# Kernel optimization log

Measured on AMD Instinct MI355X. Metric: run time of the kernel, lower is better.

The kernel has to match this reference:

```python
import jax, jax.numpy as jnp
import numpy as np

EMBED_DIM = 1024
HEAD_DIM = 64


def setup_inputs() -> dict:
    key = jax.random.key(0)
    ks = jax.random.split(key, 7)
    s_in = EMBED_DIM ** -0.5  # torch Linear default init scale
    x = jax.random.normal(ks[0], (4, 4096, EMBED_DIM), dtype=jnp.float32)
    Wk = jax.random.uniform(ks[1], (HEAD_DIM, EMBED_DIM), jnp.float32, -s_in, s_in)
    bk = jax.random.uniform(ks[2], (HEAD_DIM,), jnp.float32, -s_in, s_in)
    Wq = jax.random.uniform(ks[3], (HEAD_DIM, EMBED_DIM), jnp.float32, -s_in, s_in)
    bq = jax.random.uniform(ks[4], (HEAD_DIM,), jnp.float32, -s_in, s_in)
    Wv = jax.random.uniform(ks[5], (HEAD_DIM, EMBED_DIM), jnp.float32, -s_in, s_in)
    bv = jax.random.uniform(ks[6], (HEAD_DIM,), jnp.float32, -s_in, s_in)
    return {"x": x, "Wq": Wq, "bq": bq, "Wk": Wk, "bk": bk, "Wv": Wv, "bv": bv}


def reference(x, Wq, bq, Wk, bk, Wv, bv):
    # torch Linear: y = x @ W.T + b
    q = jnp.einsum('btc,dc->btd', x, Wq) + bq  # [B,T,D]
    k = jnp.einsum('btc,dc->btd', x, Wk) + bk
    v = jnp.einsum('btc,dc->btd', x, Wv) + bv
    scale = HEAD_DIM ** -0.5
    # NOTE: original divides by scale (multiplies by sqrt(head_dim)) -- faithful
    scores = jnp.einsum('btd,bsd->bts', q, k) / scale  # [B,T,T]
    attn_weights = jax.nn.softmax(scores, axis=-1)
    return jnp.einsum('bts,bsd->btd', attn_weights, v)
```

## Files before the change

kernel.cpp:

```cpp
#include <hip/hip_runtime.h>

#define BATCH 4
#define SEQ   4096
#define CDIM  1024
#define DDIM  64
#define NROW  (BATCH * SEQ)
#define SPA   70
#define NSPL  8

typedef _Float16 f16;
typedef _Float16 f16x8 __attribute__((ext_vector_type(8)));
typedef _Float16 f16x4 __attribute__((ext_vector_type(4)));
typedef __fp16   h16x2 __attribute__((ext_vector_type(2)));
typedef float    f32x4 __attribute__((ext_vector_type(4)));

#define MFMA32(a, b, c) __builtin_amdgcn_mfma_f32_16x16x32_f16((a), (b), (c), 0, 0, 0)
#define MFMA16(a, b, c) __builtin_amdgcn_mfma_f32_16x16x16f16((a), (b), (c), 0, 0, 0)

#define GLDS(g, l)                                                            \
  __builtin_amdgcn_global_load_lds((const __attribute__((address_space(1))) void*)(g), \
                                   (__attribute__((address_space(3))) void*)(l), 16, 0, 0)

#define QSCALE 11.5415603f

__device__ inline f16x8 cvt8(f32x4 a, f32x4 b) {
  h16x2 p0 = __builtin_amdgcn_cvt_pkrtz(a[0], a[1]);
  h16x2 p1 = __builtin_amdgcn_cvt_pkrtz(a[2], a[3]);
  h16x2 p2 = __builtin_amdgcn_cvt_pkrtz(b[0], b[1]);
  h16x2 p3 = __builtin_amdgcn_cvt_pkrtz(b[2], b[3]);
  f16x8 r;
  r[0] = p0[0]; r[1] = p0[1]; r[2] = p1[0]; r[3] = p1[1];
  r[4] = p2[0]; r[5] = p2[1]; r[6] = p3[0]; r[7] = p3[1];
  return r;
}

__device__ inline f16x4 cvt4(float a, float b, float c, float d) {
  h16x2 lo = __builtin_amdgcn_cvt_pkrtz(a, b);
  h16x2 hi = __builtin_amdgcn_cvt_pkrtz(c, d);
  f16x4 r;
  r[0] = lo[0]; r[1] = lo[1]; r[2] = hi[0]; r[3] = hi[1];
  return r;
}

__global__ __launch_bounds__(256) void prep_w_kernel(const float* __restrict__ Wq,
                                                     const float* __restrict__ Wk,
                                                     const float* __restrict__ Wv,
                                                     f16* __restrict__ wf) {
  const int i = (blockIdx.x * 256 + threadIdx.x) * 4;
  f32x4 a = *(const f32x4*)(Wq + i);
  f32x4 b = *(const f32x4*)(Wk + i);
  f32x4 c = *(const f32x4*)(Wv + i);
  *(f16x4*)(wf + i)          = cvt4(a[0], a[1], a[2], a[3]);
  *(f16x4*)(wf + 65536 + i)  = cvt4(b[0], b[1], b[2], b[3]);
  *(f16x4*)(wf + 131072 + i) = cvt4(c[0], c[1], c[2], c[3]);
}

__global__ __launch_bounds__(256, 1) void proj_kernel(const float* __restrict__ x,
                                                      const f16* __restrict__ wf,
                                                      const float* __restrict__ bq,
                                                      const float* __restrict__ bk,
                                                      const float* __restrict__ bv,
                                                      f16* __restrict__ qs,
                                                      f16* __restrict__ ks,
                                                      f16* __restrict__ vT) {
  __shared__ __attribute__((aligned(16))) float xb[2][4096];
  __shared__ __attribute__((aligned(16))) f16 wb[2][12288];
  const int tid = threadIdx.x, lane = tid & 63, w = tid >> 6;
  const int n = lane & 15, quad = lane >> 4;
  const int rowbase = blockIdx.x * 64;
  const int row0w = rowbase + w * 16;

  const float* xsrc[4];
#pragma unroll
  for (int i = 0; i < 4; ++i) {
    const int c2 = i >> 1, h = i & 1;
    xsrc[i] = x + (size_t)(row0w + n) * CDIM + c2 * 32 + quad * 8 + h * 4;
  }
  const f16* wsrc[6];
#pragma unroll
  for (int i = 0; i < 6; ++i) {
    const int e = w * 6 + i;
    const int c2e = e / 12, mt = e % 12;
    wsrc[i] = wf + (size_t)((mt >> 2) * 64 + (mt & 3) * 16 + n) * CDIM + c2e * 32 + quad * 8;
  }

  f32x4 acc[12];
#pragma unroll
  for (int t_ = 0; t_ < 12; ++t_) acc[t_] = (f32x4){0.f, 0.f, 0.f, 0.f};

  auto issue = [&](int ck, int b) {
#pragma unroll
    for (int i = 0; i < 4; ++i)
      GLDS(xsrc[i] + ck * 64, &xb[b][(w * 4 + i) * 256]);
#pragma unroll
    for (int i = 0; i < 6; ++i)
      GLDS(wsrc[i] + ck * 64, &wb[b][(w * 6 + i) * 512]);
  };

  issue(0, 0);
  __syncthreads();
  for (int ck = 0; ck < 16; ++ck) {
    const int b = ck & 1;
    if (ck + 1 < 16) issue(ck + 1, b ^ 1);
#pragma unroll
    for (int c2 = 0; c2 < 2; ++c2) {
      const f32x4 x0 = *(const f32x4*)&xb[b][(w * 4 + c2 * 2) * 256 + lane * 4];
      const f32x4 x1 = *(const f32x4*)&xb[b][(w * 4 + c2 * 2 + 1) * 256 + lane * 4];
      const f16x8 a = cvt8(x0, x1);
#pragma unroll
      for (int mt = 0; mt < 12; ++mt) {
        const f16x8 bf = *(const f16x8*)&wb[b][(c2 * 12 + mt) * 512 + lane * 8];
        acc[mt] = MFMA32(a, bf, acc[mt]);
      }
    }
    __syncthreads();
  }

  const float* bias_p[3] = {bq, bk, bv};
#pragma unroll
  for (int mat = 0; mat < 3; ++mat)
#pragma unroll
    for (int tile = 0; tile < 4; ++tile) {
      const int d = tile * 16 + n;
      const float bias = bias_p[mat][d];
      const int r0 = row0w + quad * 4;
      f32x4 a = acc[mat * 4 + tile];
      if (mat == 0) {
#pragma unroll
        for (int r = 0; r < 4; ++r)
          qs[(size_t)(r0 + r) * DDIM + d] = (f16)((a[r] + bias) * QSCALE);
      } else if (mat == 1) {
#pragma unroll
        for (int r = 0; r < 4; ++r)
          ks[(size_t)(r0 + r) * DDIM + d] = (f16)(a[r] + bias);
      } else {
        const int bb = r0 >> 12;
        const int t = r0 & (SEQ - 1);
        *(f16x4*)(vT + (size_t)(bb * 64 + d) * SEQ + t) =
            cvt4(a[0] + bias, a[1] + bias, a[2] + bias, a[3] + bias);
      }
    }
}

template <int NSPLIT>
__global__ __launch_bounds__(256, 4) void attn_kernel(const f16* __restrict__ qs,
                                                      const f16* __restrict__ ks,
                                                      const f16* __restrict__ vT,
                                                      float* __restrict__ outp,
                                                      f16* __restrict__ pacc,
                                                      float* __restrict__ pm,
                                                      float* __restrict__ pl) {
  __shared__ __attribute__((aligned(16))) f16 lk[64][SPA];
  __shared__ __attribute__((aligned(16))) f16 lv[64][SPA];
  const int tid = threadIdx.x, lane = tid & 63, w = tid >> 6;
  const int n = lane & 15, quad = lane >> 4;
  const int split = blockIdx.x % NSPLIT;
  const int rowblk = blockIdx.x / NSPLIT;
  const int row0 = rowblk * 128 + w * 32;
  const int bb = row0 >> 12;
  const int kbase = split * (SEQ / NSPLIT);
  const int NC = SEQ / NSPLIT / 64;

  const f16* kb = ks + (size_t)bb * SEQ * DDIM;
  const f16* vb = vT + (size_t)bb * DDIM * SEQ;

  const int srow = tid >> 2;
  const int scol = (tid & 3) * 16;
  const f16* kgp = kb + (size_t)(kbase + srow) * DDIM + scol;
  const f16* vgp = vb + (size_t)srow * SEQ + kbase + scol;

  f16x8 qf[2][2];
#pragma unroll
  for (int g = 0; g < 2; ++g)
#pragma unroll
    for (int hh = 0; hh < 2; ++hh)
      qf[g][hh] = *(const f16x8*)(qs + (size_t)(row0 + g * 16 + n) * DDIM + hh * 32 + quad * 8);

  f32x4 acc[2][4];
  float m[2] = {-1e30f, -1e30f}, ll[2] = {0.f, 0.f};
#pragma unroll
  for (int g = 0; g < 2; ++g)
#pragma unroll
    for (int t = 0; t < 4; ++t) acc[g][t] = (f32x4){0.f, 0.f, 0.f, 0.f};

  f16x8 kr0, kr1, vr0, vr1;
  auto gload = [&](int c) {
    const f16* kp = kgp + (size_t)c * 64 * DDIM;
    kr0 = *(const f16x8*)kp;
    kr1 = *(const f16x8*)(kp + 8);
    const f16* vp = vgp + c * 64;
    vr0 = *(const f16x8*)vp;
    vr1 = *(const f16x8*)(vp + 8);
  };

  gload(0);
  for (int c = 0; c < NC; ++c) {
    *(f16x8*)&lk[srow][scol] = kr0;
    *(f16x8*)&lk[srow][scol + 8] = kr1;
    *(f16x8*)&lv[srow][scol] = vr0;
    *(f16x8*)&lv[srow][scol + 8] = vr1;
    __syncthreads();
    if (c + 1 < NC) gload(c + 1);

    f32x4 s[2][4];
#pragma unroll
    for (int st = 0; st < 4; ++st) {
      const f16x8 klo = *(const f16x8*)&lk[st * 16 + n][quad * 8];
      const f16x8 khi = *(const f16x8*)&lk[st * 16 + n][32 + quad * 8];
#pragma unroll
      for (int g = 0; g < 2; ++g) {
        f32x4 z = (f32x4){0.f, 0.f, 0.f, 0.f};
        z = MFMA32(klo, qf[g][0], z);
        s[g][st] = MFMA32(khi, qf[g][1], z);
      }
    }

    f16x4 pq[2][4];
#pragma unroll
    for (int g = 0; g < 2; ++g) {
      f32x4 mx;
#pragma unroll
      for (int r = 0; r < 4; ++r)
        mx[r] = fmaxf(fmaxf(s[g][0][r], s[g][1][r]), fmaxf(s[g][2][r], s[g][3][r]));
      float mloc = fmaxf(fmaxf(mx[0], mx[1]), fmaxf(mx[2], mx[3]));
      mloc = fmaxf(mloc, __shfl_xor(mloc, 16));
      mloc = fmaxf(mloc, __shfl_xor(mloc, 32));
      const float mnew = fmaxf(m[g], mloc);
      const float alpha = __builtin_amdgcn_exp2f(m[g] - mnew);
      m[g] = mnew;
      float psum = 0.f;
#pragma unroll
      for (int st = 0; st < 4; ++st) {
        f32x4 p;
#pragma unroll
        for (int r = 0; r < 4; ++r) p[r] = __builtin_amdgcn_exp2f(s[g][st][r] - mnew);
        psum += (p[0] + p[1]) + (p[2] + p[3]);
        pq[g][st] = cvt4(p[0], p[1], p[2], p[3]);
      }
      ll[g] = ll[g] * alpha + psum;
#pragma unroll
      for (int t = 0; t < 4; ++t) acc[g][t] *= alpha;
    }

#pragma unroll
    for (int t = 0; t < 4; ++t)
#pragma unroll
      for (int st = 0; st < 4; ++st) {
        const f16x4 va = *(const f16x4*)&lv[t * 16 + n][st * 16 + quad * 4];
        acc[0][t] = MFMA16(va, pq[0][st], acc[0][t]);
        acc[1][t] = MFMA16(va, pq[1][st], acc[1][t]);
      }
    __syncthreads();
  }

  float lred[2];
#pragma unroll
  for (int g = 0; g < 2; ++g) {
    float l = ll[g];
    l += __shfl_xor(l, 16);
    l += __shfl_xor(l, 32);
    lred[g] = l;
  }

  if (NSPLIT == 1) {
#pragma unroll
    for (int g = 0; g < 2; ++g) {
      const float inv = 1.0f / lred[g];
      const int q = row0 + g * 16 + n;
#pragma unroll
      for (int t = 0; t < 4; ++t) {
        f32x4 o = acc[g][t];
#pragma unroll
        for (int r = 0; r < 4; ++r) o[r] *= inv;
        *(f32x4*)(outp + (size_t)q * DDIM + t * 16 + quad * 4) = o;
      }
    }
  } else {
#pragma unroll
    for (int g = 0; g < 2; ++g) {
      const int q = row0 + g * 16 + n;
#pragma unroll
      for (int t = 0; t < 4; ++t)
        *(f16x4*)(pacc + ((size_t)split * NROW + q) * DDIM + t * 16 + quad * 4) =
            cvt4(acc[g][t][0], acc[g][t][1], acc[g][t][2], acc[g][t][3]);
      if (quad == 0) {
        pm[split * NROW + q] = m[g];
        pl[split * NROW + q] = lred[g];
      }
    }
  }
}

template <int NSPLIT>
__global__ __launch_bounds__(256) void combine_kernel(const f16* __restrict__ pacc,
                                                      const float* __restrict__ pm,
                                                      const float* __restrict__ pl,
                                                      float* __restrict__ out) {
  const int idx = blockIdx.x * 256 + threadIdx.x;
  const int row = idx >> 4;
  const int c = (idx & 15) * 4;
  float mm = pm[row];
#pragma unroll
  for (int s = 1; s < NSPLIT; ++s) mm = fmaxf(mm, pm[s * NROW + row]);
  float L = 0.f;
  f32x4 o = (f32x4){0.f, 0.f, 0.f, 0.f};
#pragma unroll
  for (int s = 0; s < NSPLIT; ++s) {
    const float e = __builtin_amdgcn_exp2f(pm[s * NROW + row] - mm);
    L += pl[s * NROW + row] * e;
    const f16x4 a = *(const f16x4*)(pacc + ((size_t)s * NROW + row) * DDIM + c);
#pragma unroll
    for (int j = 0; j < 4; ++j) o[j] += (float)a[j] * e;
  }
  const float inv = 1.0f / L;
#pragma unroll
  for (int j = 0; j < 4; ++j) o[j] *= inv;
  *(f32x4*)(out + (size_t)row * DDIM + c) = o;
}

extern "C" void kernel_launch(void* const* d_in, const int* in_sizes, int n_in,
                              void* d_out, int out_size, void* d_ws, size_t ws_size,
                              hipStream_t stream) {
  const float* x  = (const float*)d_in[0];
  const float* Wq = (const float*)d_in[1];
  const float* bq = (const float*)d_in[2];
  const float* Wk = (const float*)d_in[3];
  const float* bk = (const float*)d_in[4];
  const float* Wv = (const float*)d_in[5];
  const float* bv = (const float*)d_in[6];
  float* out = (float*)d_out;

  f16* wf = (f16*)d_ws;
  f16* qs = wf + 3 * 65536;
  f16* ks = qs + (size_t)NROW * DDIM;
  f16* vT = ks + (size_t)NROW * DDIM;
  f16* pacc = vT + (size_t)NROW * DDIM;
  float* pm = (float*)(pacc + (size_t)NSPL * NROW * DDIM);
  float* pl = pm + (size_t)NSPL * NROW;
  const size_t need = (size_t)((char*)(pl + (size_t)NSPL * NROW) - (char*)d_ws);

  prep_w_kernel<<<dim3(64), dim3(256), 0, stream>>>(Wq, Wk, Wv, wf);
  proj_kernel<<<dim3(256), dim3(256), 0, stream>>>(x, wf, bq, bk, bv, qs, ks, vT);

  if (ws_size >= need) {
    attn_kernel<NSPL><<<dim3(128 * NSPL), dim3(256), 0, stream>>>(qs, ks, vT, nullptr, pacc, pm, pl);
    combine_kernel<NSPL><<<dim3(NROW * 16 / 256), dim3(256), 0, stream>>>(pacc, pm, pl, out);
  } else {
    attn_kernel<1><<<dim3(128), dim3(256), 0, stream>>>(qs, ks, vT, out, nullptr, nullptr, nullptr);
  }
}
```

Measured before the change: 170.5 us.

## Split projection K-dimension across waves and double the block count

The projection kernel now covers 32 rows per block instead of 64. The four waves split as two row groups times two halves of the reduction dimension, and the two partial accumulators are combined through shared memory at the end. The grid doubles to 512 blocks and launch bounds allow two blocks per CU, aiming for more parallelism and occupancy on the x-streaming GEMM. The cost is that each weight tile is loaded by twice as many blocks, plus an extra shared-memory reduction and sync.

```diff
diff --git a/kernel.cpp b/kernel.cpp
--- a/kernel.cpp
+++ b/kernel.cpp
@@ -55,7 +55,7 @@
   *(f16x4*)(wf + 131072 + i) = cvt4(c[0], c[1], c[2], c[3]);
 }
 
-__global__ __launch_bounds__(256, 1) void proj_kernel(const float* __restrict__ x,
+__global__ __launch_bounds__(256, 2) void proj_kernel(const float* __restrict__ x,
                                                       const f16* __restrict__ wf,
                                                       const float* __restrict__ bq,
                                                       const float* __restrict__ bk,
@@ -63,25 +63,26 @@
                                                       f16* __restrict__ qs,
                                                       f16* __restrict__ ks,
                                                       f16* __restrict__ vT) {
-  __shared__ __attribute__((aligned(16))) float xb[2][4096];
-  __shared__ __attribute__((aligned(16))) f16 wb[2][12288];
+  __shared__ __attribute__((aligned(16))) char smem[65536];
+  float(*xb)[4][512] = (float(*)[4][512])smem;
+  f16(*wb)[2][12][512] = (f16(*)[2][12][512])(smem + 16384);
+  f32x4(*comb)[64][12] = (f32x4(*)[64][12])smem;
+
   const int tid = threadIdx.x, lane = tid & 63, w = tid >> 6;
   const int n = lane & 15, quad = lane >> 4;
-  const int rowbase = blockIdx.x * 64;
-  const int row0w = rowbase + w * 16;
-
-  const float* xsrc[4];
-#pragma unroll
-  for (int i = 0; i < 4; ++i) {
-    const int c2 = i >> 1, h = i & 1;
-    xsrc[i] = x + (size_t)(row0w + n) * CDIM + c2 * 32 + quad * 8 + h * 4;
-  }
+  const int rw = w & 1;
+  const int kh = w >> 1;
+  const int row0w = blockIdx.x * 32 + rw * 16;
+
+  const float* xsrc[2];
+#pragma unroll
+  for (int h = 0; h < 2; ++h)
+    xsrc[h] = x + (size_t)(row0w + n) * CDIM + kh * 512 + quad * 8 + h * 4;
   const f16* wsrc[6];
 #pragma unroll
   for (int i = 0; i < 6; ++i) {
-    const int e = w * 6 + i;
-    const int c2e = e / 12, mt = e % 12;
-    wsrc[i] = wf + (size_t)((mt >> 2) * 64 + (mt & 3) * 16 + n) * CDIM + c2e * 32 + quad * 8;
+    const int mt = rw * 6 + i;
+    wsrc[i] = wf + (size_t)((mt >> 2) * 64 + (mt & 3) * 16 + n) * CDIM + kh * 512 + quad * 8;
   }
 
   f32x4 acc[12];
@@ -90,11 +91,11 @@
 
   auto issue = [&](int ck, int b) {
 #pragma unroll
-    for (int i = 0; i < 4; ++i)
-      GLDS(xsrc[i] + ck * 64, &xb[b][(w * 4 + i) * 256]);
+    for (int h = 0; h < 2; ++h)
+      GLDS(xsrc[h] + ck * 32, &xb[b][w][h * 256]);
 #pragma unroll
     for (int i = 0; i < 6; ++i)
-      GLDS(wsrc[i] + ck * 64, &wb[b][(w * 6 + i) * 512]);
+      GLDS(wsrc[i] + ck * 32, &wb[b][kh][rw * 6 + i][0]);
   };
 
   issue(0, 0);
@@ -102,18 +103,28 @@
   for (int ck = 0; ck < 16; ++ck) {
     const int b = ck & 1;
     if (ck + 1 < 16) issue(ck + 1, b ^ 1);
-#pragma unroll
-    for (int c2 = 0; c2 < 2; ++c2) {
-      const f32x4 x0 = *(const f32x4*)&xb[b][(w * 4 + c2 * 2) * 256 + lane * 4];
-      const f32x4 x1 = *(const f32x4*)&xb[b][(w * 4 + c2 * 2 + 1) * 256 + lane * 4];
-      const f16x8 a = cvt8(x0, x1);
-#pragma unroll
-      for (int mt = 0; mt < 12; ++mt) {
-        const f16x8 bf = *(const f16x8*)&wb[b][(c2 * 12 + mt) * 512 + lane * 8];
-        acc[mt] = MFMA32(a, bf, acc[mt]);
-      }
+    const f32x4 x0 = *(const f32x4*)&xb[b][w][lane * 4];
+    const f32x4 x1 = *(const f32x4*)&xb[b][w][256 + lane * 4];
+    const f16x8 a = cvt8(x0, x1);
+#pragma unroll
+    for (int mt = 0; mt < 12; ++mt) {
+      const f16x8 bf = *(const f16x8*)&wb[b][kh][mt][lane * 8];
+      acc[mt] = MFMA32(a, bf, acc[mt]);
     }
     __syncthreads();
+  }
+
+  if (kh == 1) {
+#pragma unroll
+    for (int t_ = 0; t_ < 12; ++t_) comb[rw][lane][t_] = acc[t_];
+  }
+  __syncthreads();
+  if (kh == 1) return;
+#pragma unroll
+  for (int t_ = 0; t_ < 12; ++t_) {
+    const f32x4 o = comb[rw][lane][t_];
+#pragma unroll
+    for (int r = 0; r < 4; ++r) acc[t_][r] += o[r];
   }
 
   const float* bias_p[3] = {bq, bk, bv};
@@ -340,7 +351,7 @@
   const size_t need = (size_t)((char*)(pl + (size_t)NSPL * NROW) - (char*)d_ws);
 
   prep_w_kernel<<<dim3(64), dim3(256), 0, stream>>>(Wq, Wk, Wv, wf);
-  proj_kernel<<<dim3(256), dim3(256), 0, stream>>>(x, wf, bq, bk, bv, qs, ks, vT);
+  proj_kernel<<<dim3(512), dim3(256), 0, stream>>>(x, wf, bq, bk, bv, qs, ks, vT);
 
   if (ws_size >= need) {
     attn_kernel<NSPL><<<dim3(128 * NSPL), dim3(256), 0, stream>>>(qs, ks, vT, nullptr, pacc, pm, pl);
```

Measured after the change: 170.1 us. Within noise of the previous version (-0.2%).

## Retile QKV projection to 32-row blocks with MFMA-fragment-ordered weights

Applied to the files above, without the earlier changes.

The weight prep kernel now writes f16 weights already in MFMA B-fragment order, so each projection wave loads one contiguous 1 KB chunk per tile. The projection kernel drops from 64 to 32 rows per block and gives each wave 3 of the 12 output tiles instead of all 12. It also uses smaller 32-column K chunks with 16 KB LDS buffers and two blocks per CU. The grid doubles to 512 blocks for better CU coverage and latency hiding, at the cost of more K-loop iterations and barriers and less x reuse per block.

```diff
diff --git a/kernel.cpp b/kernel.cpp
--- a/kernel.cpp
+++ b/kernel.cpp
@@ -45,101 +45,103 @@
 __global__ __launch_bounds__(256) void prep_w_kernel(const float* __restrict__ Wq,
                                                      const float* __restrict__ Wk,
                                                      const float* __restrict__ Wv,
-                                                     f16* __restrict__ wf) {
-  const int i = (blockIdx.x * 256 + threadIdx.x) * 4;
-  f32x4 a = *(const f32x4*)(Wq + i);
-  f32x4 b = *(const f32x4*)(Wk + i);
-  f32x4 c = *(const f32x4*)(Wv + i);
-  *(f16x4*)(wf + i)          = cvt4(a[0], a[1], a[2], a[3]);
-  *(f16x4*)(wf + 65536 + i)  = cvt4(b[0], b[1], b[2], b[3]);
-  *(f16x4*)(wf + 131072 + i) = cvt4(c[0], c[1], c[2], c[3]);
-}
-
-__global__ __launch_bounds__(256, 1) void proj_kernel(const float* __restrict__ x,
-                                                      const f16* __restrict__ wf,
+                                                     f16* __restrict__ wf2) {
+  const int t = blockIdx.x * 256 + threadIdx.x;
+  const int lane = t & 63;
+  const int s = t >> 6;
+  const int mt = s % 12, ck = s / 12;
+  const int mat = mt >> 2, tile = mt & 3;
+  const int n = lane & 15, quad = lane >> 4;
+  const float* W = (mat == 0) ? Wq : (mat == 1) ? Wk : Wv;
+  const float* src = W + (size_t)(tile * 16 + n) * CDIM + ck * 32 + quad * 8;
+  const f32x4 a = *(const f32x4*)src;
+  const f32x4 b = *(const f32x4*)(src + 4);
+  *(f16x8*)(wf2 + (size_t)t * 8) = cvt8(a, b);
+}
+
+__global__ __launch_bounds__(256, 2) void proj_kernel(const float* __restrict__ x,
+                                                      const f16* __restrict__ wf2,
                                                       const float* __restrict__ bq,
                                                       const float* __restrict__ bk,
                                                       const float* __restrict__ bv,
                                                       f16* __restrict__ qs,
                                                       f16* __restrict__ ks,
                                                       f16* __restrict__ vT) {
-  __shared__ __attribute__((aligned(16))) float xb[2][4096];
-  __shared__ __attribute__((aligned(16))) f16 wb[2][12288];
+  __shared__ __attribute__((aligned(16))) char smem[2 * 16384];
   const int tid = threadIdx.x, lane = tid & 63, w = tid >> 6;
   const int n = lane & 15, quad = lane >> 4;
-  const int rowbase = blockIdx.x * 64;
-  const int row0w = rowbase + w * 16;
-
-  const float* xsrc[4];
-#pragma unroll
-  for (int i = 0; i < 4; ++i) {
-    const int c2 = i >> 1, h = i & 1;
-    xsrc[i] = x + (size_t)(row0w + n) * CDIM + c2 * 32 + quad * 8 + h * 4;
-  }
-  const f16* wsrc[6];
-#pragma unroll
-  for (int i = 0; i < 6; ++i) {
-    const int e = w * 6 + i;
-    const int c2e = e / 12, mt = e % 12;
-    wsrc[i] = wf + (size_t)((mt >> 2) * 64 + (mt & 3) * 16 + n) * CDIM + c2e * 32 + quad * 8;
-  }
-
-  f32x4 acc[12];
-#pragma unroll
-  for (int t_ = 0; t_ < 12; ++t_) acc[t_] = (f32x4){0.f, 0.f, 0.f, 0.f};
+  const int rowbase = blockIdx.x * 32;
+
+  const float* xsl = x + (size_t)(rowbase + w * 8 + (lane >> 3)) * CDIM + (lane & 7) * 4;
+  const f16* wsl[3];
+#pragma unroll
+  for (int i = 0; i < 3; ++i)
+    wsl[i] = wf2 + (size_t)(w * 3 + i) * 512 + lane * 8;
+
+  f32x4 acc[2][3];
+#pragma unroll
+  for (int g = 0; g < 2; ++g)
+#pragma unroll
+    for (int i = 0; i < 3; ++i) acc[g][i] = (f32x4){0.f, 0.f, 0.f, 0.f};
 
   auto issue = [&](int ck, int b) {
-#pragma unroll
-    for (int i = 0; i < 4; ++i)
-      GLDS(xsrc[i] + ck * 64, &xb[b][(w * 4 + i) * 256]);
-#pragma unroll
-    for (int i = 0; i < 6; ++i)
-      GLDS(wsrc[i] + ck * 64, &wb[b][(w * 6 + i) * 512]);
+    char* base = smem + b * 16384;
+    GLDS(xsl + ck * 32, base + w * 1024);
+#pragma unroll
+    for (int i = 0; i < 3; ++i)
+      GLDS(wsl[i] + (size_t)ck * 12 * 512, base + 4096 + (w * 3 + i) * 1024);
   };
 
   issue(0, 0);
   __syncthreads();
-  for (int ck = 0; ck < 16; ++ck) {
+  for (int ck = 0; ck < 32; ++ck) {
     const int b = ck & 1;
-    if (ck + 1 < 16) issue(ck + 1, b ^ 1);
-#pragma unroll
-    for (int c2 = 0; c2 < 2; ++c2) {
-      const f32x4 x0 = *(const f32x4*)&xb[b][(w * 4 + c2 * 2) * 256 + lane * 4];
-      const f32x4 x1 = *(const f32x4*)&xb[b][(w * 4 + c2 * 2 + 1) * 256 + lane * 4];
-      const f16x8 a = cvt8(x0, x1);
-#pragma unroll
-      for (int mt = 0; mt < 12; ++mt) {
-        const f16x8 bf = *(const f16x8*)&wb[b][(c2 * 12 + mt) * 512 + lane * 8];
-        acc[mt] = MFMA32(a, bf, acc[mt]);
-      }
+    if (ck + 1 < 32) issue(ck + 1, b ^ 1);
+    const float* xb = (const float*)(smem + b * 16384);
+    const f16* wb = (const f16*)(smem + b * 16384 + 4096);
+    f16x8 a[2];
+#pragma unroll
+    for (int g = 0; g < 2; ++g) {
+      const f32x4 x0 = *(const f32x4*)(xb + (g * 16 + n) * 32 + quad * 8);
+      const f32x4 x1 = *(const f32x4*)(xb + (g * 16 + n) * 32 + quad * 8 + 4);
+      a[g] = cvt8(x0, x1);
+    }
+#pragma unroll
+    for (int i = 0; i < 3; ++i) {
+      const f16x8 bf = *(const f16x8*)(wb + (w * 3 + i) * 512 + lane * 8);
+      acc[0][i] = MFMA32(a[0], bf, acc[0][i]);
+      acc[1][i] = MFMA32(a[1], bf, acc[1][i]);
     }
     __syncthreads();
   }
 
   const float* bias_p[3] = {bq, bk, bv};
 #pragma unroll
-  for (int mat = 0; mat < 3; ++mat)
-#pragma unroll
-    for (int tile = 0; tile < 4; ++tile) {
-      const int d = tile * 16 + n;
-      const float bias = bias_p[mat][d];
-      const int r0 = row0w + quad * 4;
-      f32x4 a = acc[mat * 4 + tile];
+  for (int i = 0; i < 3; ++i) {
+    const int mt = w * 3 + i;
+    const int mat = mt >> 2, tile = mt & 3;
+    const int d = tile * 16 + n;
+    const float bias = bias_p[mat][d];
+#pragma unroll
+    for (int g = 0; g < 2; ++g) {
+      const int r0 = rowbase + g * 16 + quad * 4;
+      f32x4 aa = acc[g][i];
       if (mat == 0) {
 #pragma unroll
         for (int r = 0; r < 4; ++r)
-          qs[(size_t)(r0 + r) * DDIM + d] = (f16)((a[r] + bias) * QSCALE);
+          qs[(size_t)(r0 + r) * DDIM + d] = (f16)((aa[r] + bias) * QSCALE);
       } else if (mat == 1) {
 #pragma unroll
         for (int r = 0; r < 4; ++r)
-          ks[(size_t)(r0 + r) * DDIM + d] = (f16)(a[r] + bias);
+          ks[(size_t)(r0 + r) * DDIM + d] = (f16)(aa[r] + bias);
       } else {
         const int bb = r0 >> 12;
         const int t = r0 & (SEQ - 1);
         *(f16x4*)(vT + (size_t)(bb * 64 + d) * SEQ + t) =
-            cvt4(a[0] + bias, a[1] + bias, a[2] + bias, a[3] + bias);
-      }
-    }
+            cvt4(aa[0] + bias, aa[1] + bias, aa[2] + bias, aa[3] + bias);
+      }
+    }
+  }
 }
 
 template <int NSPLIT>
@@ -330,8 +332,8 @@
   const float* bv = (const float*)d_in[6];
   float* out = (float*)d_out;
 
-  f16* wf = (f16*)d_ws;
-  f16* qs = wf + 3 * 65536;
+  f16* wf2 = (f16*)d_ws;
+  f16* qs = wf2 + 3 * 65536;
   f16* ks = qs + (size_t)NROW * DDIM;
   f16* vT = ks + (size_t)NROW * DDIM;
   f16* pacc = vT + (size_t)NROW * DDIM;
@@ -339,8 +341,8 @@
   float* pl = pm + (size_t)NSPL * NROW;
   const size_t need = (size_t)((char*)(pl + (size_t)NSPL * NROW) - (char*)d_ws);
 
-  prep_w_kernel<<<dim3(64), dim3(256), 0, stream>>>(Wq, Wk, Wv, wf);
-  proj_kernel<<<dim3(256), dim3(256), 0, stream>>>(x, wf, bq, bk, bv, qs, ks, vT);
+  prep_w_kernel<<<dim3(96), dim3(256), 0, stream>>>(Wq, Wk, Wv, wf2);
+  proj_kernel<<<dim3(512), dim3(256), 0, stream>>>(x, wf2, bq, bk, bv, qs, ks, vT);
 
   if (ws_size >= need) {
     attn_kernel<NSPL><<<dim3(128 * NSPL), dim3(256), 0, stream>>>(qs, ks, vT, nullptr, pacc, pm, pl);
```

Result: faster. 164.7 us (-3.4%).
